# Kernel optimization log

Measured on AMD Instinct MI355X. Metric: run time of the kernel, lower is better.

## Reference

```python
import jax, jax.numpy as jnp
import numpy as np

P_SIZE = 128   # proto_size
HID = 768      # hidden_size
BATCH = 32
NREL = 16
RATIO = 0.5    # proto_emb_ratio


def setup_inputs() -> dict:
    key = jax.random.key(0)
    k1, k2, k3, k4 = jax.random.split(key, 4)
    return {
        "instance_embedding": jax.random.normal(k1, (BATCH, HID), jnp.float32),
        # small scale keeps sigmoid(p_h @ M_r @ p_t) away from hard saturation
        "relation_embedding": jax.random.normal(k2, (NREL, HID, HID), jnp.float32) * 0.02,
        "rel_label_ids": jax.random.randint(k3, (BATCH, NREL, P_SIZE), 0, P_SIZE + 1, dtype=jnp.int32),
        "labels": jnp.arange(BATCH, dtype=jnp.int32),  # distinct -> torch.unique is exact with static shapes
        "prototypes": jax.random.normal(k4, (P_SIZE, HID), jnp.float32),  # nn.Embedding weight
    }


def reference(instance_embedding, relation_embedding, rel_label_ids, labels, prototypes):
    P, H = prototypes.shape
    B, R, _ = rel_label_ids.shape

    # torch.unique(labels, return_inverse=True): sorted uniques + inverse map.
    labels_unique = jnp.sort(labels)                      # [K] (K == B, labels distinct)
    inv = jnp.argsort(jnp.argsort(labels))                # index_list (rank of each label)
    # original code: index = index_list[k] -> rel rows permuted by inverse map
    rel_k = rel_label_ids[inv]                            # [K,R,P]

    total_nonzero = jnp.sum(rel_label_ids) > 0
    batch_mask = (jnp.sum(rel_k, axis=(1, 2)) > 0)[:, None, None]   # skip if sum(rel[index])==0
    row_mask = (jnp.sum(rel_k, axis=2) > 0)[:, :, None]             # skip if sum(rel[index][i])==0
    m = (rel_k != P) & batch_mask & row_mask & total_nonzero        # [K,R,P] active entries
    mf = m.astype(prototypes.dtype)

    P0 = prototypes                                       # get_proto_embedding(): never updated inside loop
    heads = jnp.minimum(rel_k, P - 1)                     # safe gather (masked where == P)
    Ph = P0[heads]                                        # [K,R,P,H]  (largest intermediate)
    pt = P0[labels_unique]                                # [K,H]

    # sim[k,i,j] = sigmoid(P0[head] @ M_r[i] @ P0[label_k])
    v = jnp.einsum('rhg,kg->krh', relation_embedding, pt)           # [K,R,H]
    sim = jax.nn.sigmoid(jnp.einsum('krph,krh->krp', Ph, v))        # [K,R,P]

    # logits_ol init: zeros, then logits_ol[:][:][:][0] = 1.0 sets the k==0 slab to 1.0
    base = jnp.zeros((B, R, P, 2), prototypes.dtype).at[0].set(1.0)
    l1 = jnp.where(m, sim, base[..., 1])
    l0 = jnp.where(m, 1.0 - sim, base[..., 0])
    logits_ol = jnp.stack([l0, l1], axis=-1).reshape(-1, 2)         # [K*R*P, 2]
    labels_ol = m.astype(jnp.int32).reshape(-1)                     # [K*R*P]

    # proto propagation: mean over active (i,j) of P0[head] @ M_r[i]
    w = jnp.einsum('krp,krph->krh', mf, Ph)                         # [K,R,H]
    prop = jnp.einsum('krh,rhg->kg', w, relation_embedding)         # [K,H]
    n = jnp.sum(mf, axis=(1, 2))                                    # num_prop per k
    prop = prop / jnp.maximum(n, 1.0)[:, None]
    old_rows = prototypes[labels_unique]
    new_rows = RATIO * old_rows + (1.0 - RATIO) * prop
    rows = jnp.where((n > 0)[:, None], new_rows, old_rows)
    proto_embedding = prototypes.at[labels_unique].set(rows)        # scatter update (distinct rows)

    # CrossEntropyLoss (mean); 0 when all rel ids are zero (labels_ol would be None)
    logp = jax.nn.log_softmax(logits_ol, axis=-1)
    ce = -jnp.mean(jnp.take_along_axis(logp, labels_ol[:, None], axis=1))
    loss_ol = jnp.where(total_nonzero, ce, 0.0)

    # logits = -||proto - instance||^2 pairwise: [B, P]
    diff = instance_embedding[:, None, :] - proto_embedding[None, :, :]
    logits = -jnp.sum(diff * diff, axis=2)

    return logits, loss_ol, proto_embedding
```

## Files before the change

kernel.cpp:

```cpp
#include <hip/hip_runtime.h>
#include <hip/hip_bf16.h>
#include <math.h>

#define K_B 32
#define NRELD 16
#define PSZ 128
#define HID 768

using bf16x8 = __attribute__((ext_vector_type(8))) short;
using f32x4  = __attribute__((ext_vector_type(4))) float;

__device__ __forceinline__ unsigned int f2bf(float x) {
    unsigned int u = __float_as_uint(x);
    return (u + 0x7fffu + ((u >> 16) & 1u)) >> 16;
}
__device__ __forceinline__ float bf2f(unsigned short b) {
    return __uint_as_float(((unsigned int)b) << 16);
}

__global__ __launch_bounds__(192) void k_prep(
        const int* __restrict__ labels, const int* __restrict__ relIds,
        const float* __restrict__ P0,
        unsigned short* __restrict__ S_bf, unsigned short* __restrict__ P0_bf,
        unsigned short* __restrict__ P0T_bf, unsigned short* __restrict__ pt_bf,
        int* __restrict__ rowflag, int* __restrict__ cntRow,
        int* __restrict__ rowOwner_g)
{
    int bid = blockIdx.x, t = threadIdx.x;
    int k = bid >> 4, r = bid & 15;
    __shared__ int lab[32], rankS[32], luS[32], ownS[128];
    __shared__ int hist[128], redS[128];
    if (t < 32) lab[t] = labels[t];
    if (t < 128) { hist[t] = 0; ownS[t] = -1; }
    __syncthreads();
    if (t < 32) { int rk = 0; for (int j = 0; j < 32; ++j) rk += (lab[j] < lab[t]); rankS[t] = rk; }
    __syncthreads();
    if (t < 32) luS[rankS[t]] = lab[t];
    __syncthreads();
    if (t < 32) ownS[luS[t]] = t;
    __syncthreads();

    int id = 0, isv = 0;
    if (t < 128) {
        id = relIds[((size_t)rankS[k]*NRELD + r)*PSZ + t];
        isv = (id != PSZ);
        if (isv) atomicAdd(&hist[id], 1);
        redS[t] = id + (isv << 20);
    }
    __syncthreads();
    for (int off = 64; off; off >>= 1) {
        if (t < off) redS[t] += redS[t + off];
        __syncthreads();
    }
    int rowsum = redS[0] & 0xFFFFF;
    int cnt    = redS[0] >> 20;
    int rf     = (rowsum > 0);
    if (t < 128)
        S_bf[(size_t)bid*128 + t] = (unsigned short)f2bf(rf ? (float)hist[t] : 0.f);
    if (t == 0) { rowflag[bid] = rf; cntRow[bid] = cnt; }
    if (bid == 0 && t < 128) rowOwner_g[t] = ownS[t];

    if (bid < 128) {
        int p = bid;
        float4 v4 = *(const float4*)&P0[(size_t)p*HID + t*4];
        unsigned int b0 = f2bf(v4.x), b1 = f2bf(v4.y), b2 = f2bf(v4.z), b3 = f2bf(v4.w);
        uint2 d; d.x = b0 | (b1 << 16); d.y = b2 | (b3 << 16);
        *(uint2*)&P0_bf[(size_t)p*HID + t*4] = d;
        P0T_bf[(size_t)(t*4+0)*128 + p] = (unsigned short)b0;
        P0T_bf[(size_t)(t*4+1)*128 + p] = (unsigned short)b1;
        P0T_bf[(size_t)(t*4+2)*128 + p] = (unsigned short)b2;
        P0T_bf[(size_t)(t*4+3)*128 + p] = (unsigned short)b3;
        int kk = ownS[p];
        if (kk >= 0) *(uint2*)&pt_bf[(size_t)kk*HID + t*4] = d;
    }
}

__global__ __launch_bounds__(256) void k_vw(
        const float* __restrict__ rel, const unsigned short* __restrict__ pt_bf,
        const unsigned short* __restrict__ S_bf, const unsigned short* __restrict__ P0T_bf,
        unsigned short* __restrict__ v_bf, unsigned short* __restrict__ w_bf,
        float* __restrict__ prop, float* __restrict__ lossAcc)
{
    __shared__ unsigned short sh[32*768 + 64*128];
    int bid = blockIdx.x, t = threadIdx.x;
    int wave = t >> 6, lane = t & 63;

    if (bid < 192) {
        int r = bid & 15, hs = bid >> 4;
        unsigned short* ptS = sh;
        unsigned short* AS  = sh + 32*768;

        for (int i = t; i < 3072; i += 256) {
            int k = i / 96, c = i % 96;
            uint4 d = *(const uint4*)&pt_bf[(size_t)k*HID + c*8];
            *(uint4*)&ptS[k*768 + (c ^ (k & 7))*8] = d;
        }
        const int gq = (t & 31) * 4;
        const int hr = t >> 5;
        const size_t relbase = ((size_t)r*HID + hs*64) * HID;

        float4 buf[8];
        #pragma unroll
        for (int rr = 0; rr < 8; ++rr)
            buf[rr] = *(const float4*)&rel[relbase + (size_t)(hr + rr*8)*HID + gq];

        f32x4 acc[2] = {{0.f,0.f,0.f,0.f},{0.f,0.f,0.f,0.f}};
        const int arow = wave*16 + (lane & 15);

        for (int gt = 0; gt < 6; ++gt) {
            __syncthreads();
            #pragma unroll
            for (int rr = 0; rr < 8; ++rr) {
                int h_l = hr + rr*8;
                float4 v4 = buf[rr];
                int cs = (gq >> 3) ^ (h_l & 7);
                uint2 d; d.x = f2bf(v4.x) | (f2bf(v4.y) << 16);
                d.y = f2bf(v4.z) | (f2bf(v4.w) << 16);
                *(uint2*)&AS[h_l*128 + cs*8 + (gq & 4)] = d;
            }
            __syncthreads();
            if (gt < 5) {
                int gn = gt*128 + 128;
                #pragma unroll
                for (int rr = 0; rr < 8; ++rr)
                    buf[rr] = *(const float4*)&rel[relbase + (size_t)(hr + rr*8)*HID + gn + gq];
            }
            #pragma unroll
            for (int kk = 0; kk < 4; ++kk) {
                int cA = (kk*4 + (lane >> 4)) ^ (arow & 7);
                bf16x8 a = *(const bf16x8*)&AS[arow*128 + cA*8];
                #pragma unroll
                for (int nf = 0; nf < 2; ++nf) {
                    int k = nf*16 + (lane & 15);
                    int cB = (gt*16 + kk*4 + (lane >> 4)) ^ (k & 7);
                    bf16x8 b = *(const bf16x8*)&ptS[k*768 + cB*8];
                    acc[nf] = __builtin_amdgcn_mfma_f32_16x16x32_bf16(a, b, acc[nf], 0, 0, 0);
                }
            }
        }
        int h_out = hs*64 + wave*16 + (lane >> 4) * 4;
        #pragma unroll
        for (int nf = 0; nf < 2; ++nf) {
            int k = nf*16 + (lane & 15);
            uint2 d; d.x = f2bf(acc[nf][0]) | (f2bf(acc[nf][1]) << 16);
            d.y = f2bf(acc[nf][2]) | (f2bf(acc[nf][3]) << 16);
            *(uint2*)&v_bf[((size_t)k*NRELD + r)*HID + h_out] = d;
        }
    } else {
        int idx = bid - 192;
        int ms = idx / 12, ns = idx % 12;
        unsigned short* AS2 = sh;
        unsigned short* BS2 = sh + 64*128;
        if (t < 64) *(float4*)&prop[idx*256 + t*4] = float4{0.f,0.f,0.f,0.f};
        if (idx == 0 && t == 0) lossAcc[0] = 0.f;

        for (int i = t; i < 1024; i += 256) {
            int row = i >> 4, c = i & 15;
            *(uint4*)&AS2[row*128 + (c ^ (row & 7))*8] =
                *(const uint4*)&S_bf[(size_t)(ms*64 + row)*128 + c*8];
            *(uint4*)&BS2[row*128 + (c ^ (row & 7))*8] =
                *(const uint4*)&P0T_bf[(size_t)(ns*64 + row)*128 + c*8];
        }
        __syncthreads();
        f32x4 acc[4] = {{0.f,0.f,0.f,0.f},{0.f,0.f,0.f,0.f},{0.f,0.f,0.f,0.f},{0.f,0.f,0.f,0.f}};
        int arow = wave*16 + (lane & 15);
        #pragma unroll
        for (int kk = 0; kk < 4; ++kk) {
            int cA = (kk*4 + (lane >> 4)) ^ (arow & 7);
            bf16x8 a = *(const bf16x8*)&AS2[arow*128 + cA*8];
            #pragma unroll
            for (int nf = 0; nf < 4; ++nf) {
                int brow = nf*16 + (lane & 15);
                int cB = (kk*4 + (lane >> 4)) ^ (brow & 7);
                bf16x8 b = *(const bf16x8*)&BS2[brow*128 + cB*8];
                acc[nf] = __builtin_amdgcn_mfma_f32_16x16x32_bf16(a, b, acc[nf], 0, 0, 0);
            }
        }
        int kr0 = ms*64 + wave*16 + (lane >> 4) * 4;
        #pragma unroll
        for (int nf = 0; nf < 4; ++nf) {
            int h = ns*64 + nf*16 + (lane & 15);
            #pragma unroll
            for (int j = 0; j < 4; ++j)
                w_bf[(size_t)(kr0 + j)*HID + h] = (unsigned short)f2bf(acc[nf][j]);
        }
    }
}

__global__ __launch_bounds__(256) void k_prop_mfma(
        const float* __restrict__ rel, const unsigned short* __restrict__ w_bf,
        float* __restrict__ prop)
{
    int r = blockIdx.x, gs = blockIdx.y, t = threadIdx.x;
    int wave = t >> 6, lane = t & 63;
    __shared__ unsigned short WS[32*768];
    __shared__ unsigned short BS[64*128];

    for (int i = t; i < 3072; i += 256) {
        int k = i / 96, c = i % 96;
        uint4 d = *(const uint4*)&w_bf[((size_t)k*NRELD + r)*HID + c*8];
        *(uint4*)&WS[k*768 + (c ^ (k & 7))*8] = d;
    }
    const int gqq = t & 15;
    const int h4  = t >> 4;
    const size_t relb = (size_t)r*HID*HID + (size_t)gs*64;

    float4 buf[8];
    #pragma unroll
    for (int sup = 0; sup < 2; ++sup)
        #pragma unroll
        for (int rr = 0; rr < 4; ++rr)
            buf[sup*4+rr] = *(const float4*)&rel[relb + (size_t)(sup*64 + h4*4 + rr)*HID + gqq*4];

    f32x4 acc[2] = {{0.f,0.f,0.f,0.f},{0.f,0.f,0.f,0.f}};

    for (int ht = 0; ht < 6; ++ht) {
        __syncthreads();
        #pragma unroll
        for (int sup = 0; sup < 2; ++sup) {
            #pragma unroll
            for (int i = 0; i < 4; ++i) {
                int g_l = gqq*4 + i;
                int hloc = sup*64 + h4*4;
                unsigned int p0 = f2bf(((const float*)&buf[sup*4+0])[i]);
                unsigned int p1 = f2bf(((const float*)&buf[sup*4+1])[i]);
                unsigned int p2 = f2bf(((const float*)&buf[sup*4+2])[i]);
                unsigned int p3 = f2bf(((const float*)&buf[sup*4+3])[i]);
                int cs = (hloc >> 3) ^ ((g_l >> 2) & 7);
                uint2 d; d.x = p0 | (p1 << 16); d.y = p2 | (p3 << 16);
                *(uint2*)&BS[g_l*128 + cs*8 + (hloc & 4)] = d;
            }
        }
        __syncthreads();
        if (ht < 5) {
            int hn = ht*128 + 128;
            #pragma unroll
            for (int sup = 0; sup < 2; ++sup)
                #pragma unroll
                for (int rr = 0; rr < 4; ++rr)
                    buf[sup*4+rr] = *(const float4*)&rel[relb + (size_t)(hn + sup*64 + h4*4 + rr)*HID + gqq*4];
        }
        int g_l = wave*16 + (lane & 15);
        #pragma unroll
        for (int kk = 0; kk < 4; ++kk) {
            int cB = (kk*4 + (lane >> 4)) ^ ((g_l >> 2) & 7);
            bf16x8 b = *(const bf16x8*)&BS[g_l*128 + cB*8];
            #pragma unroll
            for (int mf = 0; mf < 2; ++mf) {
                int arow = mf*16 + (lane & 15);
                int cA = (ht*16 + kk*4 + (lane >> 4)) ^ (arow & 7);
                bf16x8 a = *(const bf16x8*)&WS[arow*768 + cA*8];
                acc[mf] = __builtin_amdgcn_mfma_f32_16x16x32_bf16(a, b, acc[mf], 0, 0, 0);
            }
        }
    }
    int gcol = gs*64 + wave*16 + (lane & 15);
    #pragma unroll
    for (int mf = 0; mf < 2; ++mf) {
        int k0 = mf*16 + (lane >> 4) * 4;
        #pragma unroll
        for (int j = 0; j < 4; ++j)
            atomicAdd(&prop[(size_t)(k0 + j)*HID + gcol], acc[mf][j]);
    }
}

__global__ __launch_bounds__(256) void k_zzproto(
        const unsigned short* __restrict__ v_bf, const unsigned short* __restrict__ P0_bf,
        const unsigned short* __restrict__ S_bf, float* __restrict__ lossAcc,
        const float* __restrict__ P0, const float* __restrict__ prop,
        const int* __restrict__ rowflag, const int* __restrict__ cntRow,
        const int* __restrict__ rowOwner_g, float* __restrict__ protoOut)
{
    __shared__ unsigned short sh[16*128 + 128*128];
    __shared__ float red[256];
    __shared__ float nActS[32];
    __shared__ int kS[32];
    int bid = blockIdx.x, t = threadIdx.x;
    int wave = t >> 6, lane = t & 63;

    if (bid < 32) {
        int ms = bid;
        unsigned short* AS  = sh;
        unsigned short* BS2 = sh + 16*128;
        f32x4 acc[2] = {{0.f,0.f,0.f,0.f},{0.f,0.f,0.f,0.f}};
        for (int ht = 0; ht < 6; ++ht) {
            int h0 = ht * 128;
            __syncthreads();
            {
                int row = t >> 4, c = t & 15;
                *(uint4*)&AS[row*128 + (c ^ (row & 7))*8] =
                    *(const uint4*)&v_bf[(size_t)(ms*16 + row)*HID + h0 + c*8];
                #pragma unroll
                for (int q = 0; q < 8; ++q) {
                    int j2 = t + q*256;
                    int prow = j2 >> 4, c2 = j2 & 15;
                    *(uint4*)&BS2[prow*128 + (c2 ^ (prow & 7))*8] =
                        *(const uint4*)&P0_bf[(size_t)prow*HID + h0 + c2*8];
                }
            }
            __syncthreads();
            int arow = lane & 15;
            #pragma unroll
            for (int kk = 0; kk < 4; ++kk) {
                int cA = (kk*4 + (lane >> 4)) ^ (arow & 7);
                bf16x8 a = *(const bf16x8*)&AS[arow*128 + cA*8];
                #pragma unroll
                for (int nf = 0; nf < 2; ++nf) {
                    int brow = wave*32 + nf*16 + (lane & 15);
                    int cB = (kk*4 + (lane >> 4)) ^ (brow & 7);
                    bf16x8 b = *(const bf16x8*)&BS2[brow*128 + cB*8];
                    acc[nf] = __builtin_amdgcn_mfma_f32_16x16x32_bf16(a, b, acc[nf], 0, 0, 0);
                }
            }
        }
        float term = 0.f;
        #pragma unroll
        for (int nf = 0; nf < 2; ++nf) {
            int p = wave*32 + nf*16 + (lane & 15);
            int kr0 = ms*16 + (lane >> 4) * 4;
            #pragma unroll
            for (int j = 0; j < 4; ++j) {
                float S = bf2f(S_bf[(size_t)(kr0 + j)*128 + p]);
                if (S != 0.f) {
                    float z = acc[nf][j];
                    float s = 1.f / (1.f + expf(-z));
                    term += S * (logf(expf(1.f - s) + expf(s)) - s);
                }
            }
        }
        red[t] = term;
        __syncthreads();
        for (int off = 128; off; off >>= 1) {
            if (t < off) red[t] += red[t + off];
            __syncthreads();
        }
        if (t == 0) atomicAdd(lossAcc, red[0]);
    } else {
        int base = (bid - 32) * 32;
        if (t < 32) {
            int p = base + t;
            int k = rowOwner_g[p];
            float n = 0.f;
            if (k >= 0)
                for (int i = 0; i < 16; ++i) {
                    int rr = k*NRELD + i;
                    if (rowflag[rr]) n += (float)cntRow[rr];
                }
            nActS[t] = n; kS[t] = k;
        }
        __syncthreads();
        for (int j = 0; j < 24; ++j) {
            int flat = t + 256*j;
            int pl = flat / 192, c = flat % 192;
            int p = base + pl;
            float4 old = *(const float4*)&P0[(size_t)p*HID + c*4];
            float4 o = old;
            int k = kS[pl]; float n = nActS[pl];
            if (k >= 0 && n > 0.f) {
                float4 pr = *(const float4*)&prop[(size_t)k*HID + c*4];
                float invn = 0.5f / n;
                o.x = 0.5f*old.x + pr.x*invn;
                o.y = 0.5f*old.y + pr.y*invn;
                o.z = 0.5f*old.z + pr.z*invn;
                o.w = 0.5f*old.w + pr.w*invn;
            }
            *(float4*)&protoOut[(size_t)p*HID + c*4] = o;
        }
    }
}

__global__ __launch_bounds__(128) void k_logits(const float* __restrict__ inst,
        const float* __restrict__ protoOut, const float* __restrict__ lossAcc,
        const int* __restrict__ rowflag, const int* __restrict__ cntRow,
        float* __restrict__ outLogits, float* __restrict__ outLoss)
{
    int b = blockIdx.x, t = threadIdx.x;
    __shared__ float iS[768];
    __shared__ float ls[128];
    __shared__ int ts[128];
    for (int q = 0; q < 6; ++q) iS[t + 128*q] = inst[(size_t)b*HID + t + 128*q];
    __syncthreads();
    const float4* pr = (const float4*)&protoOut[(size_t)t*HID];
    float acc = 0.f;
    for (int q = 0; q < HID/4; ++q) {
        float4 pv = pr[q];
        float dx = iS[q*4+0] - pv.x, dy = iS[q*4+1] - pv.y;
        float dz = iS[q*4+2] - pv.z, dw = iS[q*4+3] - pv.w;
        acc += dx*dx + dy*dy + dz*dz + dw*dw;
    }
    outLogits[b*PSZ + t] = -acc;
    if (b == 0) {
        float s = 0.f; int tot = 0;
        #pragma unroll
        for (int q = 0; q < 4; ++q) {
            int rr = t + 128*q;
            int rf = rowflag[rr];
            tot |= rf;
            if (rf) s += (float)cntRow[rr];
        }
        ls[t] = s; ts[t] = tot;
        __syncthreads();
        for (int off = 64; off; off >>= 1) {
            if (t < off) { ls[t] += ls[t + off]; ts[t] |= ts[t + off]; }
            __syncthreads();
        }
        if (t == 0)
            outLoss[0] = ts[0]
                ? (lossAcc[0] + (65536.f - ls[0]) * 0.6931471805599453f) * (1.f/65536.f)
                : 0.f;
    }
}

extern "C" void kernel_launch(void* const* d_in, const int* in_sizes, int n_in,
                              void* d_out, int out_size, void* d_ws, size_t ws_size,
                              hipStream_t stream)
{
    const float* inst  = (const float*)d_in[0];
    const float* rel   = (const float*)d_in[1];
    const int* relIds  = (const int*)d_in[2];
    const int* labels  = (const int*)d_in[3];
    const float* P0    = (const float*)d_in[4];
    float* out = (float*)d_out;
    float* outLogits = out;
    float* outLoss   = out + 4096;
    float* outProto  = out + 4097;

    char* ws = (char*)d_ws;
    unsigned short* v_bf    = (unsigned short*)(ws + 0);
    unsigned short* w_bf    = (unsigned short*)(ws + 786432);
    unsigned short* S_bf    = (unsigned short*)(ws + 1572864);
    unsigned short* P0_bf   = (unsigned short*)(ws + 1703936);
    unsigned short* P0T_bf  = (unsigned short*)(ws + 1900544);
    unsigned short* pt_bf   = (unsigned short*)(ws + 2097152);
    float* prop    = (float*)(ws + 2146304);
    float* lossAcc = (float*)(ws + 2244608);
    int*   rowflag = (int*)(ws + 2244736);
    int*   cntRow  = (int*)(ws + 2246784);
    int*   rowOwner= (int*)(ws + 2248832);

    k_prep<<<512, 192, 0, stream>>>(labels, relIds, P0, S_bf, P0_bf, P0T_bf,
                                    pt_bf, rowflag, cntRow, rowOwner);
    k_vw<<<288, 256, 0, stream>>>(rel, pt_bf, S_bf, P0T_bf, v_bf, w_bf,
                                  prop, lossAcc);
    k_prop_mfma<<<dim3(16,12), 256, 0, stream>>>(rel, w_bf, prop);
    k_zzproto<<<36, 256, 0, stream>>>(v_bf, P0_bf, S_bf, lossAcc, P0, prop,
                                      rowflag, cntRow, rowOwner, outProto);
    k_logits<<<32, 128, 0, stream>>>(inst, outProto, lossAcc, rowflag, cntRow,
                                     outLogits, outLoss);
}
```

Measured before the change: 136.5 us.

## Restructure pipeline into three kernels with direct w gather and split-K atomics

Computes w directly in the prep kernel by summing gathered prototype rows per relation row, which replaces the S@P0T MFMA stage and the transposed P0 copy. The v and prop matmuls are merged into one launch and split in half along the reduction dimension, with fp32 atomic accumulation, to double block count. The proto update, loss finalisation (via a done counter) and logits are fused into one tail kernel that keeps the new prototypes in LDS. This drops two launches and intermediate round trips, at the cost of atomics, uncached B-operand loads from global, and a serial 128-step gather loop per prep block.

```diff
diff --git a/kernel.cpp b/kernel.cpp
--- a/kernel.cpp
+++ b/kernel.cpp
@@ -22,16 +22,17 @@
         const int* __restrict__ labels, const int* __restrict__ relIds,
         const float* __restrict__ P0,
         unsigned short* __restrict__ S_bf, unsigned short* __restrict__ P0_bf,
-        unsigned short* __restrict__ P0T_bf, unsigned short* __restrict__ pt_bf,
+        unsigned short* __restrict__ pt_bf, unsigned short* __restrict__ w_bf,
         int* __restrict__ rowflag, int* __restrict__ cntRow,
-        int* __restrict__ rowOwner_g)
+        float* __restrict__ v_f32, float* __restrict__ prop,
+        float* __restrict__ lossAcc, int* __restrict__ done)
 {
-    int bid = blockIdx.x, t = threadIdx.x;
-    int k = bid >> 4, r = bid & 15;
+    const int bid = blockIdx.x, t = threadIdx.x;
     __shared__ int lab[32], rankS[32], luS[32], ownS[128];
-    __shared__ int hist[128], redS[128];
+    __shared__ int ids[128], hist[128], redS[192];
     if (t < 32) lab[t] = labels[t];
-    if (t < 128) { hist[t] = 0; ownS[t] = -1; }
+    if (t < 128) { ownS[t] = -1; hist[t] = 0; }
+    redS[t] = 0;
     __syncthreads();
     if (t < 32) { int rk = 0; for (int j = 0; j < 32; ++j) rk += (lab[j] < lab[t]); rankS[t] = rk; }
     __syncthreads();
@@ -40,64 +41,74 @@
     if (t < 32) ownS[luS[t]] = t;
     __syncthreads();
 
-    int id = 0, isv = 0;
-    if (t < 128) {
-        id = relIds[((size_t)rankS[k]*NRELD + r)*PSZ + t];
-        isv = (id != PSZ);
-        if (isv) atomicAdd(&hist[id], 1);
-        redS[t] = id + (isv << 20);
-    }
-    __syncthreads();
-    for (int off = 64; off; off >>= 1) {
-        if (t < off) redS[t] += redS[t + off];
-        __syncthreads();
-    }
-    int rowsum = redS[0] & 0xFFFFF;
-    int cnt    = redS[0] >> 20;
-    int rf     = (rowsum > 0);
-    if (t < 128)
-        S_bf[(size_t)bid*128 + t] = (unsigned short)f2bf(rf ? (float)hist[t] : 0.f);
-    if (t == 0) { rowflag[bid] = rf; cntRow[bid] = cnt; }
-    if (bid == 0 && t < 128) rowOwner_g[t] = ownS[t];
-
-    if (bid < 128) {
-        int p = bid;
+    if (bid < 512) {
+        int k = bid >> 4, r = bid & 15;
+        int id = PSZ, isv = 0;
+        if (t < 128) {
+            id = relIds[((size_t)rankS[k]*NRELD + r)*PSZ + t];
+            ids[t] = id;
+            isv = (id != PSZ);
+            if (isv) atomicAdd(&hist[id], 1);
+            redS[t] = id + (isv << 20);
+        }
+        __syncthreads();
+        for (int off = 64; off; off >>= 1) {
+            if (t < off) redS[t] += redS[t + off];
+            __syncthreads();
+        }
+        int rf  = ((redS[0] & 0xFFFFF) > 0);
+        int cnt = redS[0] >> 20;
+        if (t < 128) S_bf[(size_t)bid*128 + t] = (unsigned short)f2bf(rf ? (float)hist[t] : 0.f);
+        if (t == 0) { rowflag[bid] = rf; cntRow[bid] = cnt; }
+        float4 acc = {0.f, 0.f, 0.f, 0.f};
+        if (rf) {
+            for (int j = 0; j < 128; ++j) {
+                int idj = ids[j];
+                if (idj != PSZ) {
+                    float4 pv = *(const float4*)&P0[(size_t)idj*HID + t*4];
+                    acc.x += pv.x; acc.y += pv.y; acc.z += pv.z; acc.w += pv.w;
+                }
+            }
+        }
+        uint2 d; d.x = f2bf(acc.x) | (f2bf(acc.y) << 16);
+        d.y = f2bf(acc.z) | (f2bf(acc.w) << 16);
+        *(uint2*)&w_bf[(size_t)bid*HID + t*4] = d;
+    } else if (bid < 640) {
+        int p = bid - 512;
         float4 v4 = *(const float4*)&P0[(size_t)p*HID + t*4];
         unsigned int b0 = f2bf(v4.x), b1 = f2bf(v4.y), b2 = f2bf(v4.z), b3 = f2bf(v4.w);
         uint2 d; d.x = b0 | (b1 << 16); d.y = b2 | (b3 << 16);
         *(uint2*)&P0_bf[(size_t)p*HID + t*4] = d;
-        P0T_bf[(size_t)(t*4+0)*128 + p] = (unsigned short)b0;
-        P0T_bf[(size_t)(t*4+1)*128 + p] = (unsigned short)b1;
-        P0T_bf[(size_t)(t*4+2)*128 + p] = (unsigned short)b2;
-        P0T_bf[(size_t)(t*4+3)*128 + p] = (unsigned short)b3;
         int kk = ownS[p];
         if (kk >= 0) *(uint2*)&pt_bf[(size_t)kk*HID + t*4] = d;
+    } else {
+        int idx = bid - 640;
+        float4 z = {0.f, 0.f, 0.f, 0.f};
+        float4* v4p = (float4*)v_f32;
+        #pragma unroll
+        for (int q = 0; q < 4; ++q) v4p[idx*768 + q*192 + t] = z;
+        float4* p4p = (float4*)prop;
+        if (t < 48) p4p[idx*48 + t] = z;
+        if (idx == 0 && t == 0) { lossAcc[0] = 0.f; done[0] = 0; }
     }
 }
 
-__global__ __launch_bounds__(256) void k_vw(
+__global__ __launch_bounds__(256) void k_vprop(
         const float* __restrict__ rel, const unsigned short* __restrict__ pt_bf,
-        const unsigned short* __restrict__ S_bf, const unsigned short* __restrict__ P0T_bf,
-        unsigned short* __restrict__ v_bf, unsigned short* __restrict__ w_bf,
-        float* __restrict__ prop, float* __restrict__ lossAcc)
+        const unsigned short* __restrict__ w_bf,
+        float* __restrict__ v_f32, float* __restrict__ prop)
 {
-    __shared__ unsigned short sh[32*768 + 64*128];
-    int bid = blockIdx.x, t = threadIdx.x;
-    int wave = t >> 6, lane = t & 63;
-
-    if (bid < 192) {
-        int r = bid & 15, hs = bid >> 4;
-        unsigned short* ptS = sh;
-        unsigned short* AS  = sh + 32*768;
-
-        for (int i = t; i < 3072; i += 256) {
-            int k = i / 96, c = i % 96;
-            uint4 d = *(const uint4*)&pt_bf[(size_t)k*HID + c*8];
-            *(uint4*)&ptS[k*768 + (c ^ (k & 7))*8] = d;
-        }
+    __shared__ unsigned short sh[64*128];
+    const int bid = blockIdx.x, t = threadIdx.x;
+    const int wave = t >> 6, lane = t & 63;
+
+    if (bid < 384) {
+        int gh = bid / 192, rest = bid % 192;
+        int hs = rest >> 4, r = rest & 15;
+        unsigned short* AS = sh;
         const int gq = (t & 31) * 4;
         const int hr = t >> 5;
-        const size_t relbase = ((size_t)r*HID + hs*64) * HID;
+        const size_t relbase = ((size_t)r*HID + hs*64)*HID + gh*384;
 
         float4 buf[8];
         #pragma unroll
@@ -107,7 +118,7 @@
         f32x4 acc[2] = {{0.f,0.f,0.f,0.f},{0.f,0.f,0.f,0.f}};
         const int arow = wave*16 + (lane & 15);
 
-        for (int gt = 0; gt < 6; ++gt) {
+        for (int gt = 0; gt < 3; ++gt) {
             __syncthreads();
             #pragma unroll
             for (int rr = 0; rr < 8; ++rr) {
@@ -119,7 +130,7 @@
                 *(uint2*)&AS[h_l*128 + cs*8 + (gq & 4)] = d;
             }
             __syncthreads();
-            if (gt < 5) {
+            if (gt < 2) {
                 int gn = gt*128 + 128;
                 #pragma unroll
                 for (int rr = 0; rr < 8; ++rr)
@@ -132,164 +143,135 @@
                 #pragma unroll
                 for (int nf = 0; nf < 2; ++nf) {
                     int k = nf*16 + (lane & 15);
-                    int cB = (gt*16 + kk*4 + (lane >> 4)) ^ (k & 7);
-                    bf16x8 b = *(const bf16x8*)&ptS[k*768 + cB*8];
+                    bf16x8 b = *(const bf16x8*)&pt_bf[(size_t)k*HID + gh*384 + gt*128 + kk*32 + (lane >> 4)*8];
                     acc[nf] = __builtin_amdgcn_mfma_f32_16x16x32_bf16(a, b, acc[nf], 0, 0, 0);
                 }
             }
         }
-        int h_out = hs*64 + wave*16 + (lane >> 4) * 4;
+        int h_out = hs*64 + wave*16 + (lane >> 4)*4;
         #pragma unroll
         for (int nf = 0; nf < 2; ++nf) {
             int k = nf*16 + (lane & 15);
-            uint2 d; d.x = f2bf(acc[nf][0]) | (f2bf(acc[nf][1]) << 16);
-            d.y = f2bf(acc[nf][2]) | (f2bf(acc[nf][3]) << 16);
-            *(uint2*)&v_bf[((size_t)k*NRELD + r)*HID + h_out] = d;
+            #pragma unroll
+            for (int j = 0; j < 4; ++j)
+                atomicAdd(&v_f32[((size_t)k*NRELD + r)*HID + h_out + j], acc[nf][j]);
         }
     } else {
-        int idx = bid - 192;
-        int ms = idx / 12, ns = idx % 12;
-        unsigned short* AS2 = sh;
-        unsigned short* BS2 = sh + 64*128;
-        if (t < 64) *(float4*)&prop[idx*256 + t*4] = float4{0.f,0.f,0.f,0.f};
-        if (idx == 0 && t == 0) lossAcc[0] = 0.f;
-
-        for (int i = t; i < 1024; i += 256) {
-            int row = i >> 4, c = i & 15;
-            *(uint4*)&AS2[row*128 + (c ^ (row & 7))*8] =
-                *(const uint4*)&S_bf[(size_t)(ms*64 + row)*128 + c*8];
-            *(uint4*)&BS2[row*128 + (c ^ (row & 7))*8] =
-                *(const uint4*)&P0T_bf[(size_t)(ns*64 + row)*128 + c*8];
-        }
-        __syncthreads();
-        f32x4 acc[4] = {{0.f,0.f,0.f,0.f},{0.f,0.f,0.f,0.f},{0.f,0.f,0.f,0.f},{0.f,0.f,0.f,0.f}};
-        int arow = wave*16 + (lane & 15);
-        #pragma unroll
-        for (int kk = 0; kk < 4; ++kk) {
-            int cA = (kk*4 + (lane >> 4)) ^ (arow & 7);
-            bf16x8 a = *(const bf16x8*)&AS2[arow*128 + cA*8];
-            #pragma unroll
-            for (int nf = 0; nf < 4; ++nf) {
-                int brow = nf*16 + (lane & 15);
-                int cB = (kk*4 + (lane >> 4)) ^ (brow & 7);
-                bf16x8 b = *(const bf16x8*)&BS2[brow*128 + cB*8];
-                acc[nf] = __builtin_amdgcn_mfma_f32_16x16x32_bf16(a, b, acc[nf], 0, 0, 0);
-            }
-        }
-        int kr0 = ms*64 + wave*16 + (lane >> 4) * 4;
-        #pragma unroll
-        for (int nf = 0; nf < 4; ++nf) {
-            int h = ns*64 + nf*16 + (lane & 15);
+        int idx = bid - 384;
+        int hh = idx / 192, rest = idx % 192;
+        int gs = rest >> 4, r = rest & 15;
+        unsigned short* BS = sh;
+        const int gqq = t & 15;
+        const int h4  = t >> 4;
+        const size_t relb = (size_t)r*HID*HID + (size_t)gs*64 + (size_t)hh*384*HID;
+
+        float4 buf[8];
+        #pragma unroll
+        for (int sup = 0; sup < 2; ++sup)
+            #pragma unroll
+            for (int rr = 0; rr < 4; ++rr)
+                buf[sup*4+rr] = *(const float4*)&rel[relb + (size_t)(sup*64 + h4*4 + rr)*HID + gqq*4];
+
+        f32x4 acc[2] = {{0.f,0.f,0.f,0.f},{0.f,0.f,0.f,0.f}};
+
+        for (int ht = 0; ht < 3; ++ht) {
+            __syncthreads();
+            #pragma unroll
+            for (int sup = 0; sup < 2; ++sup) {
+                #pragma unroll
+                for (int i = 0; i < 4; ++i) {
+                    int g_l = gqq*4 + i;
+                    int hloc = sup*64 + h4*4;
+                    unsigned int p0 = f2bf(((const float*)&buf[sup*4+0])[i]);
+                    unsigned int p1 = f2bf(((const float*)&buf[sup*4+1])[i]);
+                    unsigned int p2 = f2bf(((const float*)&buf[sup*4+2])[i]);
+                    unsigned int p3 = f2bf(((const float*)&buf[sup*4+3])[i]);
+                    int cs = (hloc >> 3) ^ ((g_l >> 2) & 7);
+                    uint2 d; d.x = p0 | (p1 << 16); d.y = p2 | (p3 << 16);
+                    *(uint2*)&BS[g_l*128 + cs*8 + (hloc & 4)] = d;
+                }
+            }
+            __syncthreads();
+            if (ht < 2) {
+                int hn = ht*128 + 128;
+                #pragma unroll
+                for (int sup = 0; sup < 2; ++sup)
+                    #pragma unroll
+                    for (int rr = 0; rr < 4; ++rr)
+                        buf[sup*4+rr] = *(const float4*)&rel[relb + (size_t)(hn + sup*64 + h4*4 + rr)*HID + gqq*4];
+            }
+            int g_l = wave*16 + (lane & 15);
+            #pragma unroll
+            for (int kk = 0; kk < 4; ++kk) {
+                int cB = (kk*4 + (lane >> 4)) ^ ((g_l >> 2) & 7);
+                bf16x8 b = *(const bf16x8*)&BS[g_l*128 + cB*8];
+                #pragma unroll
+                for (int mf = 0; mf < 2; ++mf) {
+                    int arow = mf*16 + (lane & 15);
+                    bf16x8 a = *(const bf16x8*)&w_bf[((size_t)arow*NRELD + r)*HID + hh*384 + ht*128 + kk*32 + (lane >> 4)*8];
+                    acc[mf] = __builtin_amdgcn_mfma_f32_16x16x32_bf16(a, b, acc[mf], 0, 0, 0);
+                }
+            }
+        }
+        int gcol = gs*64 + wave*16 + (lane & 15);
+        #pragma unroll
+        for (int mf = 0; mf < 2; ++mf) {
+            int k0 = mf*16 + (lane >> 4)*4;
             #pragma unroll
             for (int j = 0; j < 4; ++j)
-                w_bf[(size_t)(kr0 + j)*HID + h] = (unsigned short)f2bf(acc[nf][j]);
+                atomicAdd(&prop[(size_t)(k0 + j)*HID + gcol], acc[mf][j]);
         }
     }
 }
 
-__global__ __launch_bounds__(256) void k_prop_mfma(
-        const float* __restrict__ rel, const unsigned short* __restrict__ w_bf,
-        float* __restrict__ prop)
-{
-    int r = blockIdx.x, gs = blockIdx.y, t = threadIdx.x;
-    int wave = t >> 6, lane = t & 63;
-    __shared__ unsigned short WS[32*768];
-    __shared__ unsigned short BS[64*128];
-
-    for (int i = t; i < 3072; i += 256) {
-        int k = i / 96, c = i % 96;
-        uint4 d = *(const uint4*)&w_bf[((size_t)k*NRELD + r)*HID + c*8];
-        *(uint4*)&WS[k*768 + (c ^ (k & 7))*8] = d;
-    }
-    const int gqq = t & 15;
-    const int h4  = t >> 4;
-    const size_t relb = (size_t)r*HID*HID + (size_t)gs*64;
-
-    float4 buf[8];
-    #pragma unroll
-    for (int sup = 0; sup < 2; ++sup)
-        #pragma unroll
-        for (int rr = 0; rr < 4; ++rr)
-            buf[sup*4+rr] = *(const float4*)&rel[relb + (size_t)(sup*64 + h4*4 + rr)*HID + gqq*4];
-
-    f32x4 acc[2] = {{0.f,0.f,0.f,0.f},{0.f,0.f,0.f,0.f}};
-
-    for (int ht = 0; ht < 6; ++ht) {
-        __syncthreads();
-        #pragma unroll
-        for (int sup = 0; sup < 2; ++sup) {
-            #pragma unroll
-            for (int i = 0; i < 4; ++i) {
-                int g_l = gqq*4 + i;
-                int hloc = sup*64 + h4*4;
-                unsigned int p0 = f2bf(((const float*)&buf[sup*4+0])[i]);
-                unsigned int p1 = f2bf(((const float*)&buf[sup*4+1])[i]);
-                unsigned int p2 = f2bf(((const float*)&buf[sup*4+2])[i]);
-                unsigned int p3 = f2bf(((const float*)&buf[sup*4+3])[i]);
-                int cs = (hloc >> 3) ^ ((g_l >> 2) & 7);
-                uint2 d; d.x = p0 | (p1 << 16); d.y = p2 | (p3 << 16);
-                *(uint2*)&BS[g_l*128 + cs*8 + (hloc & 4)] = d;
-            }
-        }
-        __syncthreads();
-        if (ht < 5) {
-            int hn = ht*128 + 128;
-            #pragma unroll
-            for (int sup = 0; sup < 2; ++sup)
-                #pragma unroll
-                for (int rr = 0; rr < 4; ++rr)
-                    buf[sup*4+rr] = *(const float4*)&rel[relb + (size_t)(hn + sup*64 + h4*4 + rr)*HID + gqq*4];
-        }
-        int g_l = wave*16 + (lane & 15);
-        #pragma unroll
-        for (int kk = 0; kk < 4; ++kk) {
-            int cB = (kk*4 + (lane >> 4)) ^ ((g_l >> 2) & 7);
-            bf16x8 b = *(const bf16x8*)&BS[g_l*128 + cB*8];
-            #pragma unroll
-            for (int mf = 0; mf < 2; ++mf) {
-                int arow = mf*16 + (lane & 15);
-                int cA = (ht*16 + kk*4 + (lane >> 4)) ^ (arow & 7);
-                bf16x8 a = *(const bf16x8*)&WS[arow*768 + cA*8];
-                acc[mf] = __builtin_amdgcn_mfma_f32_16x16x32_bf16(a, b, acc[mf], 0, 0, 0);
-            }
-        }
-    }
-    int gcol = gs*64 + wave*16 + (lane & 15);
-    #pragma unroll
-    for (int mf = 0; mf < 2; ++mf) {
-        int k0 = mf*16 + (lane >> 4) * 4;
-        #pragma unroll
-        for (int j = 0; j < 4; ++j)
-            atomicAdd(&prop[(size_t)(k0 + j)*HID + gcol], acc[mf][j]);
-    }
-}
-
-__global__ __launch_bounds__(256) void k_zzproto(
-        const unsigned short* __restrict__ v_bf, const unsigned short* __restrict__ P0_bf,
+__global__ __launch_bounds__(256) void k_tail(
+        const float* __restrict__ v_f32, const unsigned short* __restrict__ P0_bf,
         const unsigned short* __restrict__ S_bf, float* __restrict__ lossAcc,
+        int* __restrict__ done,
         const float* __restrict__ P0, const float* __restrict__ prop,
         const int* __restrict__ rowflag, const int* __restrict__ cntRow,
-        const int* __restrict__ rowOwner_g, float* __restrict__ protoOut)
+        const int* __restrict__ labels, const float* __restrict__ inst,
+        float* __restrict__ outProto, float* __restrict__ outLogits,
+        float* __restrict__ outLoss)
 {
-    __shared__ unsigned short sh[16*128 + 128*128];
-    __shared__ float red[256];
-    __shared__ float nActS[32];
-    __shared__ int kS[32];
-    int bid = blockIdx.x, t = threadIdx.x;
-    int wave = t >> 6, lane = t & 63;
+    __shared__ __align__(16) char shraw[16*772*4];
+    __shared__ int lab[32], rankS[32], luS[32], ownS[128];
+    __shared__ float redF[256];
+    __shared__ int redI[256];
+    __shared__ float nActS[16];
+    __shared__ int kS2[16];
+    const int bid = blockIdx.x, t = threadIdx.x;
+    const int wave = t >> 6, lane = t & 63;
+
+    if (t < 32) lab[t] = labels[t];
+    if (t < 128) ownS[t] = -1;
+    __syncthreads();
+    if (t < 32) { int rk = 0; for (int j = 0; j < 32; ++j) rk += (lab[j] < lab[t]); rankS[t] = rk; }
+    __syncthreads();
+    if (t < 32) luS[rankS[t]] = lab[t];
+    __syncthreads();
+    if (t < 32) ownS[luS[t]] = t;
+    __syncthreads();
 
     if (bid < 32) {
         int ms = bid;
-        unsigned short* AS  = sh;
-        unsigned short* BS2 = sh + 16*128;
+        unsigned short* AS  = (unsigned short*)shraw;
+        unsigned short* BS2 = (unsigned short*)shraw + 16*128;
         f32x4 acc[2] = {{0.f,0.f,0.f,0.f},{0.f,0.f,0.f,0.f}};
         for (int ht = 0; ht < 6; ++ht) {
             int h0 = ht * 128;
             __syncthreads();
             {
                 int row = t >> 4, c = t & 15;
-                *(uint4*)&AS[row*128 + (c ^ (row & 7))*8] =
-                    *(const uint4*)&v_bf[(size_t)(ms*16 + row)*HID + h0 + c*8];
+                const float* vp = &v_f32[(size_t)(ms*16 + row)*HID + h0 + c*8];
+                float4 a0 = *(const float4*)vp;
+                float4 a1 = *(const float4*)(vp + 4);
+                uint4 d;
+                d.x = f2bf(a0.x) | (f2bf(a0.y) << 16);
+                d.y = f2bf(a0.z) | (f2bf(a0.w) << 16);
+                d.z = f2bf(a1.x) | (f2bf(a1.y) << 16);
+                d.w = f2bf(a1.z) | (f2bf(a1.w) << 16);
+                *(uint4*)&AS[row*128 + (c ^ (row & 7))*8] = d;
                 #pragma unroll
                 for (int q = 0; q < 8; ++q) {
                     int j2 = t + q*256;
@@ -317,7 +299,7 @@
         #pragma unroll
         for (int nf = 0; nf < 2; ++nf) {
             int p = wave*32 + nf*16 + (lane & 15);
-            int kr0 = ms*16 + (lane >> 4) * 4;
+            int kr0 = ms*16 + (lane >> 4)*4;
             #pragma unroll
             for (int j = 0; j < 4; ++j) {
                 float S = bf2f(S_bf[(size_t)(kr0 + j)*128 + p]);
@@ -328,34 +310,61 @@
                 }
             }
         }
-        red[t] = term;
+        redF[t] = term;
         __syncthreads();
         for (int off = 128; off; off >>= 1) {
-            if (t < off) red[t] += red[t + off];
-            __syncthreads();
-        }
-        if (t == 0) atomicAdd(lossAcc, red[0]);
+            if (t < off) redF[t] += redF[t + off];
+            __syncthreads();
+        }
+        if (t == 0) atomicAdd(lossAcc, redF[0]);
+        __threadfence();
+        __syncthreads();
+        float s2 = 0.f; int tot = 0;
+        #pragma unroll
+        for (int q = 0; q < 2; ++q) {
+            int rr2 = t + 256*q;
+            int rf = rowflag[rr2];
+            tot |= rf;
+            if (rf) s2 += (float)cntRow[rr2];
+        }
+        redF[t] = s2; redI[t] = tot;
+        __syncthreads();
+        for (int off = 128; off; off >>= 1) {
+            if (t < off) { redF[t] += redF[t + off]; redI[t] |= redI[t + off]; }
+            __syncthreads();
+        }
+        if (t == 0) {
+            int old = atomicAdd(done, 1);
+            if (old == 31) {
+                __threadfence();
+                float cur = atomicAdd(lossAcc, 0.f);
+                outLoss[0] = redI[0]
+                    ? (cur + (65536.f - redF[0]) * 0.6931471805599453f) * (1.f/65536.f)
+                    : 0.f;
+            }
+        }
     } else {
-        int base = (bid - 32) * 32;
-        if (t < 32) {
-            int p = base + t;
-            int k = rowOwner_g[p];
+        float* protoS = (float*)shraw;
+        const int PSTR = 772;
+        int pb = (bid - 32) * 16;
+        if (t < 16) {
+            int p = pb + t;
+            int k = ownS[p];
             float n = 0.f;
             if (k >= 0)
                 for (int i = 0; i < 16; ++i) {
-                    int rr = k*NRELD + i;
-                    if (rowflag[rr]) n += (float)cntRow[rr];
-                }
-            nActS[t] = n; kS[t] = k;
-        }
-        __syncthreads();
-        for (int j = 0; j < 24; ++j) {
-            int flat = t + 256*j;
-            int pl = flat / 192, c = flat % 192;
-            int p = base + pl;
+                    int rr2 = k*NRELD + i;
+                    if (rowflag[rr2]) n += (float)cntRow[rr2];
+                }
+            nActS[t] = n; kS2[t] = k;
+        }
+        __syncthreads();
+        for (int it = t; it < 16*192; it += 256) {
+            int pl = it / 192, c = it % 192;
+            int p = pb + pl;
             float4 old = *(const float4*)&P0[(size_t)p*HID + c*4];
             float4 o = old;
-            int k = kS[pl]; float n = nActS[pl];
+            int k = kS2[pl]; float n = nActS[pl];
             if (k >= 0 && n > 0.f) {
                 float4 pr = *(const float4*)&prop[(size_t)k*HID + c*4];
                 float invn = 0.5f / n;
@@ -364,50 +373,27 @@
                 o.z = 0.5f*old.z + pr.z*invn;
                 o.w = 0.5f*old.w + pr.w*invn;
             }
-            *(float4*)&protoOut[(size_t)p*HID + c*4] = o;
-        }
-    }
-}
-
-__global__ __launch_bounds__(128) void k_logits(const float* __restrict__ inst,
-        const float* __restrict__ protoOut, const float* __restrict__ lossAcc,
-        const int* __restrict__ rowflag, const int* __restrict__ cntRow,
-        float* __restrict__ outLogits, float* __restrict__ outLoss)
-{
-    int b = blockIdx.x, t = threadIdx.x;
-    __shared__ float iS[768];
-    __shared__ float ls[128];
-    __shared__ int ts[128];
-    for (int q = 0; q < 6; ++q) iS[t + 128*q] = inst[(size_t)b*HID + t + 128*q];
-    __syncthreads();
-    const float4* pr = (const float4*)&protoOut[(size_t)t*HID];
-    float acc = 0.f;
-    for (int q = 0; q < HID/4; ++q) {
-        float4 pv = pr[q];
-        float dx = iS[q*4+0] - pv.x, dy = iS[q*4+1] - pv.y;
-        float dz = iS[q*4+2] - pv.z, dw = iS[q*4+3] - pv.w;
-        acc += dx*dx + dy*dy + dz*dz + dw*dw;
-    }
-    outLogits[b*PSZ + t] = -acc;
-    if (b == 0) {
-        float s = 0.f; int tot = 0;
-        #pragma unroll
-        for (int q = 0; q < 4; ++q) {
-            int rr = t + 128*q;
-            int rf = rowflag[rr];
-            tot |= rf;
-            if (rf) s += (float)cntRow[rr];
-        }
-        ls[t] = s; ts[t] = tot;
-        __syncthreads();
-        for (int off = 64; off; off >>= 1) {
-            if (t < off) { ls[t] += ls[t + off]; ts[t] |= ts[t + off]; }
-            __syncthreads();
-        }
-        if (t == 0)
-            outLoss[0] = ts[0]
-                ? (lossAcc[0] + (65536.f - ls[0]) * 0.6931471805599453f) * (1.f/65536.f)
-                : 0.f;
+            *(float4*)&outProto[(size_t)p*HID + c*4] = o;
+            protoS[pl*PSTR + c*4+0] = o.x;
+            protoS[pl*PSTR + c*4+1] = o.y;
+            protoS[pl*PSTR + c*4+2] = o.z;
+            protoS[pl*PSTR + c*4+3] = o.w;
+        }
+        __syncthreads();
+        int b = t & 31, p2 = (t >> 5) * 2;
+        const float4* ir = (const float4*)&inst[(size_t)b*HID];
+        float a0 = 0.f, a1 = 0.f;
+        for (int q = 0; q < HID/4; ++q) {
+            float4 iv = ir[q];
+            float4 pv0 = *(const float4*)&protoS[p2*PSTR + q*4];
+            float4 pv1 = *(const float4*)&protoS[(p2+1)*PSTR + q*4];
+            float dx = iv.x - pv0.x, dy = iv.y - pv0.y, dz = iv.z - pv0.z, dw = iv.w - pv0.w;
+            a0 += dx*dx + dy*dy + dz*dz + dw*dw;
+            dx = iv.x - pv1.x; dy = iv.y - pv1.y; dz = iv.z - pv1.z; dw = iv.w - pv1.w;
+            a1 += dx*dx + dy*dy + dz*dz + dw*dw;
+        }
+        outLogits[b*PSZ + pb + p2]     = -a0;
+        outLogits[b*PSZ + pb + p2 + 1] = -a1;
     }
 }
 
@@ -426,25 +412,22 @@
     float* outProto  = out + 4097;
 
     char* ws = (char*)d_ws;
-    unsigned short* v_bf    = (unsigned short*)(ws + 0);
-    unsigned short* w_bf    = (unsigned short*)(ws + 786432);
-    unsigned short* S_bf    = (unsigned short*)(ws + 1572864);
-    unsigned short* P0_bf   = (unsigned short*)(ws + 1703936);
-    unsigned short* P0T_bf  = (unsigned short*)(ws + 1900544);
-    unsigned short* pt_bf   = (unsigned short*)(ws + 2097152);
-    float* prop    = (float*)(ws + 2146304);
-    float* lossAcc = (float*)(ws + 2244608);
-    int*   rowflag = (int*)(ws + 2244736);
-    int*   cntRow  = (int*)(ws + 2246784);
-    int*   rowOwner= (int*)(ws + 2248832);
-
-    k_prep<<<512, 192, 0, stream>>>(labels, relIds, P0, S_bf, P0_bf, P0T_bf,
-                                    pt_bf, rowflag, cntRow, rowOwner);
-    k_vw<<<288, 256, 0, stream>>>(rel, pt_bf, S_bf, P0T_bf, v_bf, w_bf,
-                                  prop, lossAcc);
-    k_prop_mfma<<<dim3(16,12), 256, 0, stream>>>(rel, w_bf, prop);
-    k_zzproto<<<36, 256, 0, stream>>>(v_bf, P0_bf, S_bf, lossAcc, P0, prop,
-                                      rowflag, cntRow, rowOwner, outProto);
-    k_logits<<<32, 128, 0, stream>>>(inst, outProto, lossAcc, rowflag, cntRow,
-                                     outLogits, outLoss);
-}
+    float* v_f32            = (float*)(ws + 0);
+    unsigned short* w_bf    = (unsigned short*)(ws + 1572864);
+    unsigned short* S_bf    = (unsigned short*)(ws + 2359296);
+    unsigned short* P0_bf   = (unsigned short*)(ws + 2490368);
+    unsigned short* pt_bf   = (unsigned short*)(ws + 2686976);
+    float* prop    = (float*)(ws + 2736128);
+    float* lossAcc = (float*)(ws + 2834432);
+    int*   done    = (int*)(ws + 2834560);
+    int*   rowflag = (int*)(ws + 2834688);
+    int*   cntRow  = (int*)(ws + 2836736);
+
+    k_prep<<<768, 192, 0, stream>>>(labels, relIds, P0, S_bf, P0_bf, pt_bf,
+                                    w_bf, rowflag, cntRow, v_f32, prop,
+                                    lossAcc, done);
+    k_vprop<<<768, 256, 0, stream>>>(rel, pt_bf, w_bf, v_f32, prop);
+    k_tail<<<40, 256, 0, stream>>>(v_f32, P0_bf, S_bf, lossAcc, done, P0, prop,
+                                   rowflag, cntRow, labels, inst,
+                                   outProto, outLogits, outLoss);
+}
```

Result: slower. 157.2 us (+15.1%).

## Fuse proto update, logits and loss finalize into one tail kernel

Applied to the files above, without the earlier changes.

Merges the prototype-update kernel and the logits kernel into a single tail kernel. Proto-update blocks keep their 16 updated rows in shared memory and compute logits for those rows directly. The loss is finalized by the last of the 32 loss blocks, detected with an atomic done counter. This removes one launch and the global round trip of the updated prototypes, but adds a threadfence/atomic completion protocol and recomputes the label ranking in every block.

```diff
diff --git a/kernel.cpp b/kernel.cpp
--- a/kernel.cpp
+++ b/kernel.cpp
@@ -24,7 +24,7 @@
         unsigned short* __restrict__ S_bf, unsigned short* __restrict__ P0_bf,
         unsigned short* __restrict__ P0T_bf, unsigned short* __restrict__ pt_bf,
         int* __restrict__ rowflag, int* __restrict__ cntRow,
-        int* __restrict__ rowOwner_g)
+        int* __restrict__ done)
 {
     int bid = blockIdx.x, t = threadIdx.x;
     int k = bid >> 4, r = bid & 15;
@@ -49,7 +49,7 @@
     }
     __syncthreads();
     for (int off = 64; off; off >>= 1) {
-        if (t < off) redS[t] += redS[t + off];
+        if (t < off && t < 128) redS[t] += redS[t + off];
         __syncthreads();
     }
     int rowsum = redS[0] & 0xFFFFF;
@@ -58,7 +58,7 @@
     if (t < 128)
         S_bf[(size_t)bid*128 + t] = (unsigned short)f2bf(rf ? (float)hist[t] : 0.f);
     if (t == 0) { rowflag[bid] = rf; cntRow[bid] = cnt; }
-    if (bid == 0 && t < 128) rowOwner_g[t] = ownS[t];
+    if (bid == 0 && t == 0) done[0] = 0;
 
     if (bid < 128) {
         int p = bid;
@@ -89,7 +89,6 @@
         int r = bid & 15, hs = bid >> 4;
         unsigned short* ptS = sh;
         unsigned short* AS  = sh + 32*768;
-
         for (int i = t; i < 3072; i += 256) {
             int k = i / 96, c = i % 96;
             uint4 d = *(const uint4*)&pt_bf[(size_t)k*HID + c*8];
@@ -98,15 +97,12 @@
         const int gq = (t & 31) * 4;
         const int hr = t >> 5;
         const size_t relbase = ((size_t)r*HID + hs*64) * HID;
-
         float4 buf[8];
         #pragma unroll
         for (int rr = 0; rr < 8; ++rr)
             buf[rr] = *(const float4*)&rel[relbase + (size_t)(hr + rr*8)*HID + gq];
-
         f32x4 acc[2] = {{0.f,0.f,0.f,0.f},{0.f,0.f,0.f,0.f}};
         const int arow = wave*16 + (lane & 15);
-
         for (int gt = 0; gt < 6; ++gt) {
             __syncthreads();
             #pragma unroll
@@ -153,7 +149,6 @@
         unsigned short* BS2 = sh + 64*128;
         if (t < 64) *(float4*)&prop[idx*256 + t*4] = float4{0.f,0.f,0.f,0.f};
         if (idx == 0 && t == 0) lossAcc[0] = 0.f;
-
         for (int i = t; i < 1024; i += 256) {
             int row = i >> 4, c = i & 15;
             *(uint4*)&AS2[row*128 + (c ^ (row & 7))*8] =
@@ -195,7 +190,6 @@
     int wave = t >> 6, lane = t & 63;
     __shared__ unsigned short WS[32*768];
     __shared__ unsigned short BS[64*128];
-
     for (int i = t; i < 3072; i += 256) {
         int k = i / 96, c = i % 96;
         uint4 d = *(const uint4*)&w_bf[((size_t)k*NRELD + r)*HID + c*8];
@@ -204,16 +198,13 @@
     const int gqq = t & 15;
     const int h4  = t >> 4;
     const size_t relb = (size_t)r*HID*HID + (size_t)gs*64;
-
     float4 buf[8];
     #pragma unroll
     for (int sup = 0; sup < 2; ++sup)
         #pragma unroll
         for (int rr = 0; rr < 4; ++rr)
             buf[sup*4+rr] = *(const float4*)&rel[relb + (size_t)(sup*64 + h4*4 + rr)*HID + gqq*4];
-
     f32x4 acc[2] = {{0.f,0.f,0.f,0.f},{0.f,0.f,0.f,0.f}};
-
     for (int ht = 0; ht < 6; ++ht) {
         __syncthreads();
         #pragma unroll
@@ -257,31 +248,46 @@
     int gcol = gs*64 + wave*16 + (lane & 15);
     #pragma unroll
     for (int mf = 0; mf < 2; ++mf) {
-        int k0 = mf*16 + (lane >> 4) * 4;
+        int k0 = mf*16 + (lane >> 4)*4;
         #pragma unroll
         for (int j = 0; j < 4; ++j)
             atomicAdd(&prop[(size_t)(k0 + j)*HID + gcol], acc[mf][j]);
     }
 }
 
-__global__ __launch_bounds__(256) void k_zzproto(
+__global__ __launch_bounds__(256) void k_tail(
         const unsigned short* __restrict__ v_bf, const unsigned short* __restrict__ P0_bf,
         const unsigned short* __restrict__ S_bf, float* __restrict__ lossAcc,
+        int* __restrict__ done,
         const float* __restrict__ P0, const float* __restrict__ prop,
         const int* __restrict__ rowflag, const int* __restrict__ cntRow,
-        const int* __restrict__ rowOwner_g, float* __restrict__ protoOut)
+        const int* __restrict__ labels, const float* __restrict__ inst,
+        float* __restrict__ outProto, float* __restrict__ outLogits,
+        float* __restrict__ outLoss)
 {
-    __shared__ unsigned short sh[16*128 + 128*128];
-    __shared__ float red[256];
-    __shared__ float nActS[32];
-    __shared__ int kS[32];
-    int bid = blockIdx.x, t = threadIdx.x;
-    int wave = t >> 6, lane = t & 63;
+    __shared__ __align__(16) char shraw[16*772*4];
+    __shared__ int lab[32], rankS[32], luS[32], ownS[128];
+    __shared__ float redF[256];
+    __shared__ int redI[256];
+    __shared__ float nActS[16];
+    __shared__ int kS2[16];
+    const int bid = blockIdx.x, t = threadIdx.x;
+    const int wave = t >> 6, lane = t & 63;
+
+    if (t < 32) lab[t] = labels[t];
+    if (t < 128) ownS[t] = -1;
+    __syncthreads();
+    if (t < 32) { int rk = 0; for (int j = 0; j < 32; ++j) rk += (lab[j] < lab[t]); rankS[t] = rk; }
+    __syncthreads();
+    if (t < 32) luS[rankS[t]] = lab[t];
+    __syncthreads();
+    if (t < 32) ownS[luS[t]] = t;
+    __syncthreads();
 
     if (bid < 32) {
         int ms = bid;
-        unsigned short* AS  = sh;
-        unsigned short* BS2 = sh + 16*128;
+        unsigned short* AS  = (unsigned short*)shraw;
+        unsigned short* BS2 = (unsigned short*)shraw + 16*128;
         f32x4 acc[2] = {{0.f,0.f,0.f,0.f},{0.f,0.f,0.f,0.f}};
         for (int ht = 0; ht < 6; ++ht) {
             int h0 = ht * 128;
@@ -317,7 +323,7 @@
         #pragma unroll
         for (int nf = 0; nf < 2; ++nf) {
             int p = wave*32 + nf*16 + (lane & 15);
-            int kr0 = ms*16 + (lane >> 4) * 4;
+            int kr0 = ms*16 + (lane >> 4)*4;
             #pragma unroll
             for (int j = 0; j < 4; ++j) {
                 float S = bf2f(S_bf[(size_t)(kr0 + j)*128 + p]);
@@ -328,34 +334,61 @@
                 }
             }
         }
-        red[t] = term;
+        redF[t] = term;
         __syncthreads();
         for (int off = 128; off; off >>= 1) {
-            if (t < off) red[t] += red[t + off];
-            __syncthreads();
-        }
-        if (t == 0) atomicAdd(lossAcc, red[0]);
+            if (t < off) redF[t] += redF[t + off];
+            __syncthreads();
+        }
+        if (t == 0) atomicAdd(lossAcc, redF[0]);
+        __threadfence();
+        __syncthreads();
+        float s2 = 0.f; int tot = 0;
+        #pragma unroll
+        for (int q = 0; q < 2; ++q) {
+            int rr2 = t + 256*q;
+            int rf = rowflag[rr2];
+            tot |= rf;
+            if (rf) s2 += (float)cntRow[rr2];
+        }
+        redF[t] = s2; redI[t] = tot;
+        __syncthreads();
+        for (int off = 128; off; off >>= 1) {
+            if (t < off) { redF[t] += redF[t + off]; redI[t] |= redI[t + off]; }
+            __syncthreads();
+        }
+        if (t == 0) {
+            int old = atomicAdd(done, 1);
+            if (old == 31) {
+                __threadfence();
+                float cur = atomicAdd(lossAcc, 0.f);
+                outLoss[0] = redI[0]
+                    ? (cur + (65536.f - redF[0]) * 0.6931471805599453f) * (1.f/65536.f)
+                    : 0.f;
+            }
+        }
     } else {
-        int base = (bid - 32) * 32;
-        if (t < 32) {
-            int p = base + t;
-            int k = rowOwner_g[p];
+        float* protoS = (float*)shraw;
+        const int PSTR = 772;
+        int pb = (bid - 32) * 16;
+        if (t < 16) {
+            int p = pb + t;
+            int k = ownS[p];
             float n = 0.f;
             if (k >= 0)
                 for (int i = 0; i < 16; ++i) {
-                    int rr = k*NRELD + i;
-                    if (rowflag[rr]) n += (float)cntRow[rr];
+                    int rr2 = k*NRELD + i;
+                    if (rowflag[rr2]) n += (float)cntRow[rr2];
                 }
-            nActS[t] = n; kS[t] = k;
-        }
-        __syncthreads();
-        for (int j = 0; j < 24; ++j) {
-            int flat = t + 256*j;
-            int pl = flat / 192, c = flat % 192;
-            int p = base + pl;
+            nActS[t] = n; kS2[t] = k;
+        }
+        __syncthreads();
+        for (int it = t; it < 16*192; it += 256) {
+            int pl = it / 192, c = it % 192;
+            int p = pb + pl;
             float4 old = *(const float4*)&P0[(size_t)p*HID + c*4];
             float4 o = old;
-            int k = kS[pl]; float n = nActS[pl];
+            int k = kS2[pl]; float n = nActS[pl];
             if (k >= 0 && n > 0.f) {
                 float4 pr = *(const float4*)&prop[(size_t)k*HID + c*4];
                 float invn = 0.5f / n;
@@ -364,50 +397,27 @@
                 o.z = 0.5f*old.z + pr.z*invn;
                 o.w = 0.5f*old.w + pr.w*invn;
             }
-            *(float4*)&protoOut[(size_t)p*HID + c*4] = o;
-        }
-    }
-}
-
-__global__ __launch_bounds__(128) void k_logits(const float* __restrict__ inst,
-        const float* __restrict__ protoOut, const float* __restrict__ lossAcc,
-        const int* __restrict__ rowflag, const int* __restrict__ cntRow,
-        float* __restrict__ outLogits, float* __restrict__ outLoss)
-{
-    int b = blockIdx.x, t = threadIdx.x;
-    __shared__ float iS[768];
-    __shared__ float ls[128];
-    __shared__ int ts[128];
-    for (int q = 0; q < 6; ++q) iS[t + 128*q] = inst[(size_t)b*HID + t + 128*q];
-    __syncthreads();
-    const float4* pr = (const float4*)&protoOut[(size_t)t*HID];
-    float acc = 0.f;
-    for (int q = 0; q < HID/4; ++q) {
-        float4 pv = pr[q];
-        float dx = iS[q*4+0] - pv.x, dy = iS[q*4+1] - pv.y;
-        float dz = iS[q*4+2] - pv.z, dw = iS[q*4+3] - pv.w;
-        acc += dx*dx + dy*dy + dz*dz + dw*dw;
-    }
-    outLogits[b*PSZ + t] = -acc;
-    if (b == 0) {
-        float s = 0.f; int tot = 0;
-        #pragma unroll
-        for (int q = 0; q < 4; ++q) {
-            int rr = t + 128*q;
-            int rf = rowflag[rr];
-            tot |= rf;
-            if (rf) s += (float)cntRow[rr];
-        }
-        ls[t] = s; ts[t] = tot;
-        __syncthreads();
-        for (int off = 64; off; off >>= 1) {
-            if (t < off) { ls[t] += ls[t + off]; ts[t] |= ts[t + off]; }
-            __syncthreads();
-        }
-        if (t == 0)
-            outLoss[0] = ts[0]
-                ? (lossAcc[0] + (65536.f - ls[0]) * 0.6931471805599453f) * (1.f/65536.f)
-                : 0.f;
+            *(float4*)&outProto[(size_t)p*HID + c*4] = o;
+            protoS[pl*PSTR + c*4+0] = o.x;
+            protoS[pl*PSTR + c*4+1] = o.y;
+            protoS[pl*PSTR + c*4+2] = o.z;
+            protoS[pl*PSTR + c*4+3] = o.w;
+        }
+        __syncthreads();
+        int b = t & 31, p2 = (t >> 5) * 2;
+        const float4* ir = (const float4*)&inst[(size_t)b*HID];
+        float a0 = 0.f, a1 = 0.f;
+        for (int q = 0; q < HID/4; ++q) {
+            float4 iv = ir[q];
+            float4 pv0 = *(const float4*)&protoS[p2*PSTR + q*4];
+            float4 pv1 = *(const float4*)&protoS[(p2+1)*PSTR + q*4];
+            float dx = iv.x - pv0.x, dy = iv.y - pv0.y, dz = iv.z - pv0.z, dw = iv.w - pv0.w;
+            a0 += dx*dx + dy*dy + dz*dz + dw*dw;
+            dx = iv.x - pv1.x; dy = iv.y - pv1.y; dz = iv.z - pv1.z; dw = iv.w - pv1.w;
+            a1 += dx*dx + dy*dy + dz*dz + dw*dw;
+        }
+        outLogits[b*PSZ + pb + p2]     = -a0;
+        outLogits[b*PSZ + pb + p2 + 1] = -a1;
     }
 }
 
@@ -434,17 +444,16 @@
     unsigned short* pt_bf   = (unsigned short*)(ws + 2097152);
     float* prop    = (float*)(ws + 2146304);
     float* lossAcc = (float*)(ws + 2244608);
-    int*   rowflag = (int*)(ws + 2244736);
-    int*   cntRow  = (int*)(ws + 2246784);
-    int*   rowOwner= (int*)(ws + 2248832);
+    int*   done    = (int*)(ws + 2244736);
+    int*   rowflag = (int*)(ws + 2244864);
+    int*   cntRow  = (int*)(ws + 2246912);
 
     k_prep<<<512, 192, 0, stream>>>(labels, relIds, P0, S_bf, P0_bf, P0T_bf,
-                                    pt_bf, rowflag, cntRow, rowOwner);
+                                    pt_bf, rowflag, cntRow, done);
     k_vw<<<288, 256, 0, stream>>>(rel, pt_bf, S_bf, P0T_bf, v_bf, w_bf,
                                   prop, lossAcc);
     k_prop_mfma<<<dim3(16,12), 256, 0, stream>>>(rel, w_bf, prop);
-    k_zzproto<<<36, 256, 0, stream>>>(v_bf, P0_bf, S_bf, lossAcc, P0, prop,
-                                      rowflag, cntRow, rowOwner, outProto);
-    k_logits<<<32, 128, 0, stream>>>(inst, outProto, lossAcc, rowflag, cntRow,
-                                     outLogits, outLoss);
-}
+    k_tail<<<40, 256, 0, stream>>>(v_bf, P0_bf, S_bf, lossAcc, done, P0, prop,
+                                   rowflag, cntRow, labels, inst,
+                                   outProto, outLogits, outLoss);
+}
```

New measurement: 137.0 us. About the same (+0.4%).
